# Optimization experiments

Hardware: AMD Instinct MI355X
Metric: run time of the kernel (lower is better)

The kernel has to match this reference:

```python
import jax, jax.numpy as jnp
import numpy as np

DIM_X, DIM_Y, BATCH = 64, 64, 2


def setup_inputs() -> dict:
    key = jax.random.key(0)
    k1, k2, k3 = jax.random.split(key, 3)
    mean_in = jax.random.normal(k1, (BATCH, DIM_X, DIM_Y), dtype=jnp.float32)
    # std must be positive
    std_in = jax.random.uniform(k2, (BATCH, DIM_X, DIM_Y), dtype=jnp.float32, minval=0.1, maxval=1.0)
    # identity correlation matrix -> PSD covariance, valid sqrt/div downstream
    n = DIM_X * DIM_Y
    corr_in = jnp.broadcast_to(jnp.eye(n, dtype=jnp.float32), (BATCH, n, n))
    # kaiming_uniform_(a=sqrt(5)) on a (dx, dy) weight -> bound = 1/sqrt(dy)
    bound = 1.0 / np.sqrt(DIM_Y)
    weight = jax.random.uniform(k3, (DIM_X, DIM_Y), dtype=jnp.float32, minval=-bound, maxval=bound)
    return {"mean_in": mean_in, "std_in": std_in, "corr_in": corr_in, "weight": weight}


def reference(mean_in, std_in, corr_in, weight):
    B, dx, dy = mean_in.shape
    n = dx * dy
    # fft(fft(w, dim=0), dim=1) == 2D FFT
    wfft = jnp.fft.fft2(weight)  # (dx, dy) complex

    # covariance from std and corr: cov[b,i,j,k,l] = std[b,i,j] * corr[b,i,j,k,l] * std[b,k,l]
    corr = corr_in.reshape(B, dx, dy, dx, dy)
    cov = std_in[:, None, None, :, :] * corr * std_in[:, :, :, None, None]

    # mean path: circular 2D convolution via FFT
    mean_fft = jnp.fft.fft2(mean_in, axes=(1, 2))
    mean_out = jnp.real(jnp.fft.ifft2(wfft[None] * mean_fft, axes=(1, 2)))

    # covariance path: 4D FFT, broadcast multiply by wfft on both index pairs, 4D IFFT
    cov_f = jnp.fft.fftn(cov, axes=(1, 2, 3, 4))
    cov_f = wfft[None, None, None, :, :] * cov_f * wfft[None, :, :, None, None]
    cov_out = jnp.real(jnp.fft.ifftn(cov_f, axes=(1, 2, 3, 4)))
    cov_out = cov_out.reshape(B, n, n)

    # update_correlation: std = sqrt(diag(cov)); corr = cov / (std outer std)
    var = jnp.diagonal(cov_out, axis1=-2, axis2=-1)  # (B, n)
    std_out = jnp.sqrt(jnp.maximum(var, 1e-12))
    denom = std_out[:, :, None] * std_out[:, None, :]
    corr_out = cov_out / denom
    std_out = std_out.reshape(B, dx, dy)
    return mean_out, std_out, corr_out
```

## Files before the change

### kernel.cpp

```cpp
#include <hip/hip_runtime.h>
#include <math.h>

#define DXY   64
#define NN    4096
#define NB    2
#define CP    65

#define C16 0.9238795325112867f
#define S16 0.3826834323650898f
#define R22 0.7071067811865476f

__device__ __forceinline__ void cmul_ip(float2& a, float wr, float wi) {
    float t = a.x * wr - a.y * wi;
    a.y = a.x * wi + a.y * wr;
    a.x = t;
}

__device__ __forceinline__ void bf4(float2* y, int i0, int i1, int i2, int i3, int inv) {
    float2 a0 = y[i0], a1 = y[i1], a2 = y[i2], a3 = y[i3];
    float t0r = a0.x + a2.x, t0i = a0.y + a2.y;
    float t1r = a0.x - a2.x, t1i = a0.y - a2.y;
    float t2r = a1.x + a3.x, t2i = a1.y + a3.y;
    float dr  = a1.x - a3.x, di  = a1.y - a3.y;
    float t3r, t3i;
    if (inv) { t3r = -di; t3i = dr; } else { t3r = di; t3i = -dr; }
    y[i0] = make_float2(t0r + t2r, t0i + t2i);
    y[i1] = make_float2(t1r + t3r, t1i + t3i);
    y[i2] = make_float2(t0r - t2r, t0i - t2i);
    y[i3] = make_float2(t1r - t3r, t1i - t3i);
}

__device__ __forceinline__ void fft16_fwd(float2* y) {
    bf4(y, 0, 4, 8, 12, 0);
    bf4(y, 1, 5, 9, 13, 0);
    cmul_ip(y[5],  C16, -S16); cmul_ip(y[9],  R22, -R22); cmul_ip(y[13],  S16, -C16);
    bf4(y, 2, 6, 10, 14, 0);
    cmul_ip(y[6],  R22, -R22); cmul_ip(y[10], 0.f, -1.f); cmul_ip(y[14], -R22, -R22);
    bf4(y, 3, 7, 11, 15, 0);
    cmul_ip(y[7],  S16, -C16); cmul_ip(y[11], -R22, -R22); cmul_ip(y[15], -C16,  S16);
    bf4(y, 0, 1, 2, 3, 0); bf4(y, 4, 5, 6, 7, 0);
    bf4(y, 8, 9, 10, 11, 0); bf4(y, 12, 13, 14, 15, 0);
}

__device__ __forceinline__ void fft16_inv(float2* y) {
    bf4(y, 0, 1, 2, 3, 1); bf4(y, 4, 5, 6, 7, 1);
    bf4(y, 8, 9, 10, 11, 1); bf4(y, 12, 13, 14, 15, 1);
    cmul_ip(y[5],  C16,  S16); cmul_ip(y[9],  R22,  R22); cmul_ip(y[13],  S16,  C16);
    cmul_ip(y[6],  R22,  R22); cmul_ip(y[10], 0.f,  1.f); cmul_ip(y[14], -R22,  R22);
    cmul_ip(y[7],  S16,  C16); cmul_ip(y[11], -R22,  R22); cmul_ip(y[15], -C16, -S16);
    bf4(y, 0, 4, 8, 12, 1); bf4(y, 1, 5, 9, 13, 1);
    bf4(y, 2, 6, 10, 14, 1); bf4(y, 3, 7, 11, 15, 1);
}

template<int US, int NS, bool FUSEW>
__device__ void fwd_pass(float2* z, const float2* __restrict__ wf, int u, int k1,
                         float c1r, float c1i, float s2, float2 Wb)
{
    const int B = u * US;
    float2 y[16];
    float twr = 1.f, twi = 0.f;
#pragma unroll
    for (int n2 = 0; n2 < 16; ++n2) {
        float2 x0 = z[B + n2 * NS];
        float2 x1 = z[B + (n2 + 16) * NS];
        float2 x2 = z[B + (n2 + 32) * NS];
        float2 x3 = z[B + (n2 + 48) * NS];
        float er  = fmaf(s2, x2.x, x0.x), ei = fmaf(s2, x2.y, x0.y);
        float orr = fmaf(s2, x3.x, x1.x), oi = fmaf(s2, x3.y, x1.y);
        float br = er + c1r * orr - c1i * oi;
        float bi = ei + c1r * oi + c1i * orr;
        y[n2].x = twr * br - twi * bi;
        y[n2].y = twr * bi + twi * br;
        float t = twr * Wb.x - twi * Wb.y;
        twi = twr * Wb.y + twi * Wb.x;
        twr = t;
    }
    fft16_fwd(y);
    if (FUSEW) {
#pragma unroll
        for (int p = 0; p < 16; ++p) {
            float2 wv = wf[(16 * k1 + p) * 64 + u];
            cmul_ip(y[p], wv.x, wv.y);
        }
    }
    __syncthreads();
#pragma unroll
    for (int p = 0; p < 16; ++p) z[B + (16 * k1 + p) * NS] = y[p];
    __syncthreads();
}

template<int US, int NS>
__device__ void inv_pass(float2* z, int u, int k1,
                         float ci1r, float ci1i, float s2, float2 Wbc)
{
    const int B = u * US;
    float2 y[16];
#pragma unroll
    for (int p = 0; p < 16; ++p) y[p] = z[B + (16 * k1 + p) * NS];
    fft16_inv(y);
    float twr = 1.f, twi = 0.f;
#pragma unroll
    for (int n2 = 0; n2 < 16; ++n2) {
        cmul_ip(y[n2], twr, twi);
        float t = twr * Wbc.x - twi * Wbc.y;
        twi = twr * Wbc.y + twi * Wbc.x;
        twr = t;
    }
#pragma unroll
    for (int n2 = 0; n2 < 16; ++n2) z[B + (16 * k1 + n2) * NS] = y[n2];
    __syncthreads();
    float2 xx[16];
#pragma unroll
    for (int n2 = 0; n2 < 16; ++n2) {
        float2 h0 = z[B + n2 * NS];
        float2 h1 = z[B + (n2 + 16) * NS];
        float2 h2 = z[B + (n2 + 32) * NS];
        float2 h3 = z[B + (n2 + 48) * NS];
        float er  = fmaf(s2, h2.x, h0.x), ei = fmaf(s2, h2.y, h0.y);
        float orr = fmaf(s2, h3.x, h1.x), oi = fmaf(s2, h3.y, h1.y);
        xx[n2].x = er + ci1r * orr - ci1i * oi;
        xx[n2].y = ei + ci1r * oi + ci1i * orr;
    }
    __syncthreads();
#pragma unroll
    for (int n2 = 0; n2 < 16; ++n2) z[B + (16 * k1 + n2) * NS] = xx[n2];
    __syncthreads();
}

__global__ __launch_bounds__(256, 4)
void row_conv2_kernel(const float* __restrict__ in, float* __restrict__ out,
                      const float2* __restrict__ wfft_br,
                      const float* __restrict__ sstd,
                      const float* __restrict__ rstd)
{
    __shared__ float2 z[64 * CP];
    const int tid = threadIdx.x;
    const int u   = ((tid >> 6) << 4) | (tid & 15);
    const int k1  = (tid >> 4) & 3;
    const float c1r = (k1 == 0) ? 1.f : ((k1 == 2) ? -1.f : 0.f);
    const float c1i = (k1 == 1) ? -1.f : ((k1 == 3) ? 1.f : 0.f);
    const float s2  = (k1 & 1) ? -1.f : 1.f;
    const float ang = -0.09817477042468103f * (float)k1;
    const float2 Wb  = make_float2(cosf(ang), sinf(ang));
    const float2 Wbc = make_float2(Wb.x, -Wb.y);
    const float ci1r = c1r, ci1i = -c1i;

    const int row0 = 2 * blockIdx.x;
    const long long off0 = (long long)row0 * NN, off1 = off0 + NN;
    const int b   = row0 >> 12;
    const int rI0 = row0 & (NN - 1), rI1 = rI0 + 1;
    const float* sb = nullptr;
    float sI0 = 1.f, sI1 = 1.f;
    if (sstd) { sb = sstd + (long long)b * NN; sI0 = sb[rI0]; sI1 = sb[rI1]; }

    float4 a4[4], c4[4], s4[4];
#pragma unroll
    for (int i = 0; i < 4; ++i) {
        int p = (tid + 256 * i) * 4;
        a4[i] = *(const float4*)(in + off0 + p);
        c4[i] = *(const float4*)(in + off1 + p);
    }
    if (sb) {
#pragma unroll
        for (int i = 0; i < 4; ++i) {
            int p = (tid + 256 * i) * 4;
            s4[i] = *(const float4*)(sb + p);
        }
    }
#pragma unroll
    for (int i = 0; i < 4; ++i) {
        int p = (tid + 256 * i) * 4;
        int r = p >> 6, c = p & 63;
        float4 a = a4[i], cc = c4[i];
        if (sb) {
            float4 s = s4[i];
            a.x *= sI0 * s.x; a.y *= sI0 * s.y; a.z *= sI0 * s.z; a.w *= sI0 * s.w;
            cc.x *= sI1 * s.x; cc.y *= sI1 * s.y; cc.z *= sI1 * s.z; cc.w *= sI1 * s.w;
        }
        float2* zp = z + r * CP + c;
        zp[0] = make_float2(a.x, cc.x);
        zp[1] = make_float2(a.y, cc.y);
        zp[2] = make_float2(a.z, cc.z);
        zp[3] = make_float2(a.w, cc.w);
    }
    __syncthreads();

    fwd_pass<CP, 1, false>(z, nullptr,  u, k1, c1r, c1i, s2, Wb);
    fwd_pass<1, CP, true >(z, wfft_br,  u, k1, c1r, c1i, s2, Wb);
    inv_pass<1, CP>(z, u, k1, ci1r, ci1i, s2, Wbc);
    inv_pass<CP, 1>(z, u, k1, ci1r, ci1i, s2, Wbc);

    const float scale = 1.0f / 4096.0f;
    float s0 = scale, s1 = scale;
    const float* rsb = nullptr;
    if (rstd) {
        rsb = rstd + (long long)b * NN;
        s0 *= rsb[rI0];
        s1 *= rsb[rI1];
    }
#pragma unroll
    for (int i = 0; i < 4; ++i) {
        int idx = tid + 256 * i;
        int p = idx * 4;
        int r = p >> 6, c = p & 63;
        const float2* zp = z + r * CP + c;
        float4 a, cc;
        a.x = zp[0].x; a.y = zp[1].x; a.z = zp[2].x; a.w = zp[3].x;
        cc.x = zp[0].y; cc.y = zp[1].y; cc.z = zp[2].y; cc.w = zp[3].y;
        if (rsb) {
            float4 rc = *(const float4*)(rsb + p);
            a.x *= s0 * rc.x; a.y *= s0 * rc.y; a.z *= s0 * rc.z; a.w *= s0 * rc.w;
            cc.x *= s1 * rc.x; cc.y *= s1 * rc.y; cc.z *= s1 * rc.z; cc.w *= s1 * rc.w;
        } else {
            a.x *= s0; a.y *= s0; a.z *= s0; a.w *= s0;
            cc.x *= s1; cc.y *= s1; cc.z *= s1; cc.w *= s1;
        }
        *(float4*)(out + off0 + p) = a;
        *(float4*)(out + off1 + p) = cc;
    }
}

__global__ __launch_bounds__(256, 4)
void wfft_kernel(const float* __restrict__ w, float2* wfft_br)
{
    __shared__ float2 z[64 * CP];
    const int tid = threadIdx.x;
    const int u   = ((tid >> 6) << 4) | (tid & 15);
    const int k1  = (tid >> 4) & 3;
    const float c1r = (k1 == 0) ? 1.f : ((k1 == 2) ? -1.f : 0.f);
    const float c1i = (k1 == 1) ? -1.f : ((k1 == 3) ? 1.f : 0.f);
    const float s2  = (k1 & 1) ? -1.f : 1.f;
    const float ang = -0.09817477042468103f * (float)k1;
    const float2 Wb = make_float2(cosf(ang), sinf(ang));

#pragma unroll
    for (int i = 0; i < 16; ++i) {
        int p = tid + 256 * i;
        z[(p >> 6) * CP + (p & 63)] = make_float2(w[p], 0.f);
    }
    __syncthreads();
    fwd_pass<CP, 1, false>(z, nullptr, u, k1, c1r, c1i, s2, Wb);
    fwd_pass<1, CP, false>(z, nullptr, u, k1, c1r, c1i, s2, Wb);
#pragma unroll
    for (int i = 0; i < 16; ++i) {
        int p = tid + 256 * i;
        wfft_br[p] = z[(p >> 6) * CP + (p & 63)];
    }
}

__global__ __launch_bounds__(256, 4)
void transpose_inplace_kernel(float* data, const float* __restrict__ weight,
                              float* __restrict__ var)
{
    int bx = blockIdx.x, by = blockIdx.y, b = blockIdx.z;
    if (by > bx) return;
    __shared__ float tA[64 * 65];
    __shared__ float tB[64 * 65];
    __shared__ float wAs[64], wBs[64];
    __shared__ float red[512];
    const int tid = threadIdx.x;
    const int f  = tid & 15;
    const int r0 = tid >> 4;
    long long base = (long long)b * NN * NN;
    float* A  = data + base + (long long)(by * 64) * NN + bx * 64;
    float* Bt = data + base + (long long)(bx * 64) * NN + by * 64;

    if (tid < 64)       wAs[tid]      = weight[(((bx - by) & 63) << 6) + tid];
    else if (tid < 128) wBs[tid - 64] = weight[(((by - bx) & 63) << 6) + (tid - 64)];

    const int c = tid & 63, q = tid >> 6;

    if (bx == by) {
        float4 va[4];
#pragma unroll
        for (int it = 0; it < 4; ++it) {
            int r = r0 + 16 * it;
            va[it] = *(const float4*)(A + (long long)r * NN + 4 * f);
        }
#pragma unroll
        for (int it = 0; it < 4; ++it) {
            int r = r0 + 16 * it;
            tA[(4 * f + 0) * 65 + r] = va[it].x; tA[(4 * f + 1) * 65 + r] = va[it].y;
            tA[(4 * f + 2) * 65 + r] = va[it].z; tA[(4 * f + 3) * 65 + r] = va[it].w;
        }
        __syncthreads();
        float4 ov[4];
#pragma unroll
        for (int it = 0; it < 4; ++it) {
            int cc = r0 + 16 * it;
            ov[it].x = tA[cc * 65 + 4 * f + 0]; ov[it].y = tA[cc * 65 + 4 * f + 1];
            ov[it].z = tA[cc * 65 + 4 * f + 2]; ov[it].w = tA[cc * 65 + 4 * f + 3];
        }
        float sA = 0.f;
#pragma unroll
        for (int k = 0; k < 16; ++k) {
            int r = q * 16 + k;
            sA = fmaf(wAs[(c - r) & 63], tA[c * 65 + r], sA);
        }
        red[tid] = sA;
        __syncthreads();
        if (tid < 64) {
            float v = red[tid] + red[tid + 64] + red[tid + 128] + red[tid + 192];
            atomicAdd(&var[(long long)b * NN + bx * 64 + tid], v);
        }
#pragma unroll
        for (int it = 0; it < 4; ++it) {
            int cc = r0 + 16 * it;
            *(float4*)(A + (long long)cc * NN + 4 * f) = ov[it];
        }
    } else {
        float4 va[4], wb[4];
#pragma unroll
        for (int it = 0; it < 4; ++it) {
            int r = r0 + 16 * it;
            va[it] = *(const float4*)(A  + (long long)r * NN + 4 * f);
            wb[it] = *(const float4*)(Bt + (long long)r * NN + 4 * f);
        }
#pragma unroll
        for (int it = 0; it < 4; ++it) {
            int r = r0 + 16 * it;
            tA[(4 * f + 0) * 65 + r] = va[it].x; tA[(4 * f + 1) * 65 + r] = va[it].y;
            tA[(4 * f + 2) * 65 + r] = va[it].z; tA[(4 * f + 3) * 65 + r] = va[it].w;
            tB[(4 * f + 0) * 65 + r] = wb[it].x; tB[(4 * f + 1) * 65 + r] = wb[it].y;
            tB[(4 * f + 2) * 65 + r] = wb[it].z; tB[(4 * f + 3) * 65 + r] = wb[it].w;
        }
        __syncthreads();
        float4 ov[4], ow[4];
#pragma unroll
        for (int it = 0; it < 4; ++it) {
            int cc = r0 + 16 * it;
            ov[it].x = tB[cc * 65 + 4 * f + 0]; ov[it].y = tB[cc * 65 + 4 * f + 1];
            ov[it].z = tB[cc * 65 + 4 * f + 2]; ov[it].w = tB[cc * 65 + 4 * f + 3];
            ow[it].x = tA[cc * 65 + 4 * f + 0]; ow[it].y = tA[cc * 65 + 4 * f + 1];
            ow[it].z = tA[cc * 65 + 4 * f + 2]; ow[it].w = tA[cc * 65 + 4 * f + 3];
        }
        float sA = 0.f, sB = 0.f;
#pragma unroll
        for (int k = 0; k < 16; ++k) {
            int r = q * 16 + k;
            sA = fmaf(wAs[(c - r) & 63], tA[c * 65 + r], sA);
            sB = fmaf(wBs[(c - r) & 63], tB[c * 65 + r], sB);
        }
        red[tid] = sA; red[256 + tid] = sB;
        __syncthreads();
        if (tid < 64) {
            float v = red[tid] + red[tid + 64] + red[tid + 128] + red[tid + 192];
            atomicAdd(&var[(long long)b * NN + bx * 64 + tid], v);
        } else if (tid < 128) {
            int t = tid - 64;
            float v = red[256 + t] + red[320 + t] + red[384 + t] + red[448 + t];
            atomicAdd(&var[(long long)b * NN + by * 64 + t], v);
        }
#pragma unroll
        for (int it = 0; it < 4; ++it) {
            int cc = r0 + 16 * it;
            *(float4*)(A  + (long long)cc * NN + 4 * f) = ov[it];
            *(float4*)(Bt + (long long)cc * NN + 4 * f) = ow[it];
        }
    }
}

__global__ __launch_bounds__(256)
void std_kernel(const float* __restrict__ var, float* std_out, float* rstd, int n)
{
    int i = blockIdx.x * 256 + threadIdx.x;
    if (i < n) {
        float s = sqrtf(fmaxf(var[i], 1e-12f));
        std_out[i] = s;
        rstd[i] = 1.0f / s;
    }
}

extern "C" void kernel_launch(void* const* d_in, const int* in_sizes, int n_in,
                              void* d_out, int out_size, void* d_ws, size_t ws_size,
                              hipStream_t stream)
{
    const float* mean_in = (const float*)d_in[0];
    const float* std_in  = (const float*)d_in[1];
    const float* corr_in = (const float*)d_in[2];
    const float* weight  = (const float*)d_in[3];

    float* out      = (float*)d_out;
    float* mean_out = out;
    float* std_out  = out + 8192;
    float* corr_out = out + 16384;

    float*  ws      = (float*)d_ws;
    float2* wfft_br = (float2*)ws;
    float*  var_ws  = ws + 8192;
    float*  rstd_ws = ws + 16384;

    hipMemsetAsync(var_ws, 0, NB * NN * sizeof(float), stream);

    wfft_kernel<<<1, 256, 0, stream>>>(weight, wfft_br);

    row_conv2_kernel<<<1, 256, 0, stream>>>(mean_in, mean_out, wfft_br,
                                            nullptr, nullptr);

    row_conv2_kernel<<<NB * NN / 2, 256, 0, stream>>>(corr_in, corr_out, wfft_br,
                                                      std_in, nullptr);

    dim3 tg(64, 64, NB);
    transpose_inplace_kernel<<<tg, 256, 0, stream>>>(corr_out, weight, var_ws);

    std_kernel<<<(NB * NN + 255) / 256, 256, 0, stream>>>(var_ws, std_out,
                                                          rstd_ws, NB * NN);

    row_conv2_kernel<<<NB * NN / 2, 256, 0, stream>>>(corr_out, corr_out, wfft_br,
                                                      nullptr, rstd_ws);
}
```

Measured before the change: 443.1 us.

## Swizzle FFT shared layout, fold mean conv and memset into existing kernels

Replaces the padded 65-stride shared-memory layout with an unpadded 4096-entry XOR-swizzled layout, which shrinks LDS per block and lets launch bounds target 5 blocks per CU. The separate single-block mean convolution launch is folded into the corr row-conv grid as an extra block. The memset of the variance workspace moves into the wfft kernel. This removes two launches and aims to raise occupancy, at the cost of extra index arithmetic for the swizzle and some register pressure from the higher occupancy target.

```diff
diff --git a/kernel.cpp b/kernel.cpp
--- a/kernel.cpp
+++ b/kernel.cpp
@@ -4,11 +4,16 @@
 #define DXY   64
 #define NN    4096
 #define NB    2
-#define CP    65
 
 #define C16 0.9238795325112867f
 #define S16 0.3826834323650898f
 #define R22 0.7071067811865476f
+
+template<int AX>
+__device__ __forceinline__ int zix(int l, int e) {
+    return (AX == 0) ? ((l << 6) | (e ^ (l & 15)))
+                     : ((e << 6) | (l ^ (e & 15)));
+}
 
 __device__ __forceinline__ void cmul_ip(float2& a, float wr, float wi) {
     float t = a.x * wr - a.y * wi;
@@ -52,19 +57,18 @@
     bf4(y, 2, 6, 10, 14, 1); bf4(y, 3, 7, 11, 15, 1);
 }
 
-template<int US, int NS, bool FUSEW>
+template<int AX, bool FUSEW>
 __device__ void fwd_pass(float2* z, const float2* __restrict__ wf, int u, int k1,
                          float c1r, float c1i, float s2, float2 Wb)
 {
-    const int B = u * US;
     float2 y[16];
     float twr = 1.f, twi = 0.f;
 #pragma unroll
     for (int n2 = 0; n2 < 16; ++n2) {
-        float2 x0 = z[B + n2 * NS];
-        float2 x1 = z[B + (n2 + 16) * NS];
-        float2 x2 = z[B + (n2 + 32) * NS];
-        float2 x3 = z[B + (n2 + 48) * NS];
+        float2 x0 = z[zix<AX>(u, n2)];
+        float2 x1 = z[zix<AX>(u, n2 + 16)];
+        float2 x2 = z[zix<AX>(u, n2 + 32)];
+        float2 x3 = z[zix<AX>(u, n2 + 48)];
         float er  = fmaf(s2, x2.x, x0.x), ei = fmaf(s2, x2.y, x0.y);
         float orr = fmaf(s2, x3.x, x1.x), oi = fmaf(s2, x3.y, x1.y);
         float br = er + c1r * orr - c1i * oi;
@@ -85,18 +89,17 @@
     }
     __syncthreads();
 #pragma unroll
-    for (int p = 0; p < 16; ++p) z[B + (16 * k1 + p) * NS] = y[p];
-    __syncthreads();
-}
-
-template<int US, int NS>
+    for (int p = 0; p < 16; ++p) z[zix<AX>(u, 16 * k1 + p)] = y[p];
+    __syncthreads();
+}
+
+template<int AX>
 __device__ void inv_pass(float2* z, int u, int k1,
                          float ci1r, float ci1i, float s2, float2 Wbc)
 {
-    const int B = u * US;
     float2 y[16];
 #pragma unroll
-    for (int p = 0; p < 16; ++p) y[p] = z[B + (16 * k1 + p) * NS];
+    for (int p = 0; p < 16; ++p) y[p] = z[zix<AX>(u, 16 * k1 + p)];
     fft16_inv(y);
     float twr = 1.f, twi = 0.f;
 #pragma unroll
@@ -107,15 +110,15 @@
         twr = t;
     }
 #pragma unroll
-    for (int n2 = 0; n2 < 16; ++n2) z[B + (16 * k1 + n2) * NS] = y[n2];
+    for (int n2 = 0; n2 < 16; ++n2) z[zix<AX>(u, 16 * k1 + n2)] = y[n2];
     __syncthreads();
     float2 xx[16];
 #pragma unroll
     for (int n2 = 0; n2 < 16; ++n2) {
-        float2 h0 = z[B + n2 * NS];
-        float2 h1 = z[B + (n2 + 16) * NS];
-        float2 h2 = z[B + (n2 + 32) * NS];
-        float2 h3 = z[B + (n2 + 48) * NS];
+        float2 h0 = z[zix<AX>(u, n2)];
+        float2 h1 = z[zix<AX>(u, n2 + 16)];
+        float2 h2 = z[zix<AX>(u, n2 + 32)];
+        float2 h3 = z[zix<AX>(u, n2 + 48)];
         float er  = fmaf(s2, h2.x, h0.x), ei = fmaf(s2, h2.y, h0.y);
         float orr = fmaf(s2, h3.x, h1.x), oi = fmaf(s2, h3.y, h1.y);
         xx[n2].x = er + ci1r * orr - ci1i * oi;
@@ -123,17 +126,19 @@
     }
     __syncthreads();
 #pragma unroll
-    for (int n2 = 0; n2 < 16; ++n2) z[B + (16 * k1 + n2) * NS] = xx[n2];
-    __syncthreads();
-}
-
-__global__ __launch_bounds__(256, 4)
+    for (int n2 = 0; n2 < 16; ++n2) z[zix<AX>(u, 16 * k1 + n2)] = xx[n2];
+    __syncthreads();
+}
+
+__global__ __launch_bounds__(256, 5)
 void row_conv2_kernel(const float* __restrict__ in, float* __restrict__ out,
                       const float2* __restrict__ wfft_br,
                       const float* __restrict__ sstd,
-                      const float* __restrict__ rstd)
-{
-    __shared__ float2 z[64 * CP];
+                      const float* __restrict__ rstd,
+                      const float* __restrict__ mean_i,
+                      float* __restrict__ mean_o)
+{
+    __shared__ float2 z[4096];
     const int tid = threadIdx.x;
     const int u   = ((tid >> 6) << 4) | (tid & 15);
     const int k1  = (tid >> 4) & 3;
@@ -145,20 +150,29 @@
     const float2 Wbc = make_float2(Wb.x, -Wb.y);
     const float ci1r = c1r, ci1i = -c1i;
 
-    const int row0 = 2 * blockIdx.x;
+    const float* ip = in;
+    float*       op = out;
+    const float* sstdp = sstd;
+    const float* rstdp = rstd;
+    int bid = blockIdx.x;
+    if (mean_i && bid == (int)gridDim.x - 1) {
+        ip = mean_i; op = mean_o; sstdp = nullptr; rstdp = nullptr; bid = 0;
+    }
+
+    const int row0 = 2 * bid;
     const long long off0 = (long long)row0 * NN, off1 = off0 + NN;
     const int b   = row0 >> 12;
     const int rI0 = row0 & (NN - 1), rI1 = rI0 + 1;
     const float* sb = nullptr;
     float sI0 = 1.f, sI1 = 1.f;
-    if (sstd) { sb = sstd + (long long)b * NN; sI0 = sb[rI0]; sI1 = sb[rI1]; }
+    if (sstdp) { sb = sstdp + (long long)b * NN; sI0 = sb[rI0]; sI1 = sb[rI1]; }
 
     float4 a4[4], c4[4], s4[4];
 #pragma unroll
     for (int i = 0; i < 4; ++i) {
         int p = (tid + 256 * i) * 4;
-        a4[i] = *(const float4*)(in + off0 + p);
-        c4[i] = *(const float4*)(in + off1 + p);
+        a4[i] = *(const float4*)(ip + off0 + p);
+        c4[i] = *(const float4*)(ip + off1 + p);
     }
     if (sb) {
 #pragma unroll
@@ -177,24 +191,23 @@
             a.x *= sI0 * s.x; a.y *= sI0 * s.y; a.z *= sI0 * s.z; a.w *= sI0 * s.w;
             cc.x *= sI1 * s.x; cc.y *= sI1 * s.y; cc.z *= sI1 * s.z; cc.w *= sI1 * s.w;
         }
-        float2* zp = z + r * CP + c;
-        zp[0] = make_float2(a.x, cc.x);
-        zp[1] = make_float2(a.y, cc.y);
-        zp[2] = make_float2(a.z, cc.z);
-        zp[3] = make_float2(a.w, cc.w);
-    }
-    __syncthreads();
-
-    fwd_pass<CP, 1, false>(z, nullptr,  u, k1, c1r, c1i, s2, Wb);
-    fwd_pass<1, CP, true >(z, wfft_br,  u, k1, c1r, c1i, s2, Wb);
-    inv_pass<1, CP>(z, u, k1, ci1r, ci1i, s2, Wbc);
-    inv_pass<CP, 1>(z, u, k1, ci1r, ci1i, s2, Wbc);
+        z[zix<0>(r, c + 0)] = make_float2(a.x, cc.x);
+        z[zix<0>(r, c + 1)] = make_float2(a.y, cc.y);
+        z[zix<0>(r, c + 2)] = make_float2(a.z, cc.z);
+        z[zix<0>(r, c + 3)] = make_float2(a.w, cc.w);
+    }
+    __syncthreads();
+
+    fwd_pass<0, false>(z, nullptr,  u, k1, c1r, c1i, s2, Wb);
+    fwd_pass<1, true >(z, wfft_br,  u, k1, c1r, c1i, s2, Wb);
+    inv_pass<1>(z, u, k1, ci1r, ci1i, s2, Wbc);
+    inv_pass<0>(z, u, k1, ci1r, ci1i, s2, Wbc);
 
     const float scale = 1.0f / 4096.0f;
     float s0 = scale, s1 = scale;
     const float* rsb = nullptr;
-    if (rstd) {
-        rsb = rstd + (long long)b * NN;
+    if (rstdp) {
+        rsb = rstdp + (long long)b * NN;
         s0 *= rsb[rI0];
         s1 *= rsb[rI1];
     }
@@ -203,10 +216,13 @@
         int idx = tid + 256 * i;
         int p = idx * 4;
         int r = p >> 6, c = p & 63;
-        const float2* zp = z + r * CP + c;
+        float2 z0 = z[zix<0>(r, c + 0)];
+        float2 z1 = z[zix<0>(r, c + 1)];
+        float2 z2 = z[zix<0>(r, c + 2)];
+        float2 z3 = z[zix<0>(r, c + 3)];
         float4 a, cc;
-        a.x = zp[0].x; a.y = zp[1].x; a.z = zp[2].x; a.w = zp[3].x;
-        cc.x = zp[0].y; cc.y = zp[1].y; cc.z = zp[2].y; cc.w = zp[3].y;
+        a.x = z0.x; a.y = z1.x; a.z = z2.x; a.w = z3.x;
+        cc.x = z0.y; cc.y = z1.y; cc.z = z2.y; cc.w = z3.y;
         if (rsb) {
             float4 rc = *(const float4*)(rsb + p);
             a.x *= s0 * rc.x; a.y *= s0 * rc.y; a.z *= s0 * rc.z; a.w *= s0 * rc.w;
@@ -215,16 +231,19 @@
             a.x *= s0; a.y *= s0; a.z *= s0; a.w *= s0;
             cc.x *= s1; cc.y *= s1; cc.z *= s1; cc.w *= s1;
         }
-        *(float4*)(out + off0 + p) = a;
-        *(float4*)(out + off1 + p) = cc;
+        *(float4*)(op + off0 + p) = a;
+        *(float4*)(op + off1 + p) = cc;
     }
 }
 
 __global__ __launch_bounds__(256, 4)
-void wfft_kernel(const float* __restrict__ w, float2* wfft_br)
-{
-    __shared__ float2 z[64 * CP];
+void wfft_kernel(const float* __restrict__ w, float2* wfft_br,
+                 float* __restrict__ var_zero)
+{
+    __shared__ float2 z[4096];
     const int tid = threadIdx.x;
+#pragma unroll
+    for (int i = 0; i < 32; ++i) var_zero[tid + 256 * i] = 0.f;
     const int u   = ((tid >> 6) << 4) | (tid & 15);
     const int k1  = (tid >> 4) & 3;
     const float c1r = (k1 == 0) ? 1.f : ((k1 == 2) ? -1.f : 0.f);
@@ -236,15 +255,15 @@
 #pragma unroll
     for (int i = 0; i < 16; ++i) {
         int p = tid + 256 * i;
-        z[(p >> 6) * CP + (p & 63)] = make_float2(w[p], 0.f);
-    }
-    __syncthreads();
-    fwd_pass<CP, 1, false>(z, nullptr, u, k1, c1r, c1i, s2, Wb);
-    fwd_pass<1, CP, false>(z, nullptr, u, k1, c1r, c1i, s2, Wb);
+        z[zix<0>(p >> 6, p & 63)] = make_float2(w[p], 0.f);
+    }
+    __syncthreads();
+    fwd_pass<0, false>(z, nullptr, u, k1, c1r, c1i, s2, Wb);
+    fwd_pass<1, false>(z, nullptr, u, k1, c1r, c1i, s2, Wb);
 #pragma unroll
     for (int i = 0; i < 16; ++i) {
         int p = tid + 256 * i;
-        wfft_br[p] = z[(p >> 6) * CP + (p & 63)];
+        wfft_br[p] = z[zix<0>(p >> 6, p & 63)];
     }
 }
 
@@ -390,15 +409,10 @@
     float*  var_ws  = ws + 8192;
     float*  rstd_ws = ws + 16384;
 
-    hipMemsetAsync(var_ws, 0, NB * NN * sizeof(float), stream);
-
-    wfft_kernel<<<1, 256, 0, stream>>>(weight, wfft_br);
-
-    row_conv2_kernel<<<1, 256, 0, stream>>>(mean_in, mean_out, wfft_br,
-                                            nullptr, nullptr);
-
-    row_conv2_kernel<<<NB * NN / 2, 256, 0, stream>>>(corr_in, corr_out, wfft_br,
-                                                      std_in, nullptr);
+    wfft_kernel<<<1, 256, 0, stream>>>(weight, wfft_br, var_ws);
+
+    row_conv2_kernel<<<NB * NN / 2 + 1, 256, 0, stream>>>(
+        corr_in, corr_out, wfft_br, std_in, nullptr, mean_in, mean_out);
 
     dim3 tg(64, 64, NB);
     transpose_inplace_kernel<<<tg, 256, 0, stream>>>(corr_out, weight, var_ws);
@@ -406,6 +420,6 @@
     std_kernel<<<(NB * NN + 255) / 256, 256, 0, stream>>>(var_ws, std_out,
                                                           rstd_ws, NB * NN);
 
-    row_conv2_kernel<<<NB * NN / 2, 256, 0, stream>>>(corr_out, corr_out, wfft_br,
-                                                      nullptr, rstd_ws);
-}
+    row_conv2_kernel<<<NB * NN / 2, 256, 0, stream>>>(
+        corr_out, corr_out, wfft_br, nullptr, rstd_ws, nullptr, nullptr);
+}
```

Measured after the change: 552.3 us. +24.6%, slower.
